# Kernel tuning notes

Hardware: AMD Instinct MI355X
Metric: run time of the kernel (lower is better)

The kernel has to match this reference:

```python
import jax, jax.numpy as jnp
import numpy as np

HUGE = jnp.float32(1e31)   # ops.HUGE_INT
EPS = 1e-20
B, AN = 1024, 256
D = 256            # emb_dim
HD = 512           # history_dim
AD = 2 * D         # action_dim
NE, NR = 100000, 400


def setup_inputs() -> dict:
    key = jax.random.key(0)
    ks = jax.random.split(key, 12)
    e = jax.random.randint(ks[0], (B,), 0, NE)
    q = jax.random.randint(ks[1], (B,), 0, NR)
    hstate = jax.random.normal(ks[2], (B, HD), dtype=jnp.float32)
    r_space = jax.random.randint(ks[3], (B, AN), 0, NR)
    e_space = jax.random.randint(ks[4], (B, AN), 0, NE)
    # binary action mask; guarantee at least one valid action per row
    action_mask = (jax.random.uniform(ks[5], (B, AN)) > 0.2).astype(jnp.float32)
    action_mask = action_mask.at[:, 0].set(1.0)
    entity_emb = jax.random.normal(ks[6], (NE, D), dtype=jnp.float32) * 0.02
    relation_emb = jax.random.normal(ks[7], (NR, D), dtype=jnp.float32) * 0.02
    W1 = jax.random.normal(ks[8], (2 * D + HD, AD), dtype=jnp.float32) * (1.0 / np.sqrt(2 * D + HD))
    b1 = jnp.zeros((AD,), dtype=jnp.float32)
    W2 = jax.random.normal(ks[9], (AD, AD), dtype=jnp.float32) * (1.0 / np.sqrt(AD))
    b2 = jnp.zeros((AD,), dtype=jnp.float32)
    return {"e": e, "q": q, "hstate": hstate, "r_space": r_space,
            "e_space": e_space, "action_mask": action_mask,
            "entity_emb": entity_emb, "relation_emb": relation_emb,
            "W1": W1, "b1": b1, "W2": W2, "b2": b2}


def reference(e, q, hstate, r_space, e_space, action_mask,
              entity_emb, relation_emb, W1, b1, W2, b2):
    Q = relation_emb[q]                       # [B, D]
    E = entity_emb[e]                         # [B, D]
    X = jnp.concatenate([E, hstate, Q], axis=-1)          # [B, 2D+HD]
    X = jax.nn.relu(X @ W1 + b1)                          # [B, AD]
    X2 = X @ W2 + b2                                      # [B, AD]
    # action embeddings: [rel_emb[r]; ent_emb[e]] per padded action slot
    A = jnp.concatenate([relation_emb[r_space], entity_emb[e_space]], axis=-1)  # [B, AN, AD]
    scores = jnp.einsum('bad,bd->ba', A, X2) - (1.0 - action_mask) * HUGE      # [B, AN]
    action_dist = jax.nn.softmax(scores, axis=-1)
    entropy = -jnp.sum(action_dist * jnp.log(jnp.clip(action_dist, EPS)), axis=-1)  # [B]
    return action_dist, entropy
```

## Files before the change

kernel.cpp:

```cpp
#include <hip/hip_runtime.h>
#include <math.h>

#define NB   1024
#define NACT 256
#define DIM  256
#define HDIM 512
#define ADIM 512
#define KTOT 1024
#define NE   100000
#define NR   400
#define NRP  448
#define NCAT 704

typedef __attribute__((ext_vector_type(8))) short bf16x8;
typedef __attribute__((ext_vector_type(4))) float f32x4;

__device__ __forceinline__ unsigned short f2bf(float f) {
    unsigned int u = __float_as_uint(f);
    u += 0x7FFF + ((u >> 16) & 1);
    return (unsigned short)(u >> 16);
}
__device__ __forceinline__ ushort4 cvt4(float4 v) {
    ushort4 o = {f2bf(v.x), f2bf(v.y), f2bf(v.z), f2bf(v.w)};
    return o;
}

__global__ __launch_bounds__(256) void prep_kernel(
    const float* __restrict__ W1, const float* __restrict__ W2,
    const float* __restrict__ rel, const float* __restrict__ b2,
    ushort* __restrict__ W1T, ushort* __restrict__ Bcat,
    ushort* __restrict__ W2lowbf, ushort* __restrict__ relbf,
    float* __restrict__ cvec)
{
    const int blk = blockIdx.x, tid = threadIdx.x;
    if (blk < 160) {
        __shared__ float t[64][68];
        const float* in; ushort* out; int Kd, k0, n0, rowbase;
        if (blk < 128) {
            in = W1; out = W1T; Kd = 1024;
            k0 = (blk >> 3) * 64; n0 = (blk & 7) * 64; rowbase = n0;
        } else {
            const int l = blk - 128;
            in = W2; out = Bcat; Kd = 512;
            k0 = (l >> 2) * 64; n0 = 256 + (l & 3) * 64; rowbase = n0 - 256;
        }
        const int kr = tid >> 2, c = tid & 3;
        #pragma unroll
        for (int j = 0; j < 4; ++j) {
            const float4 v = *(const float4*)(in + (size_t)(k0 + kr) * ADIM + n0 + c * 16 + j * 4);
            *(float4*)&t[kr][c * 16 + j * 4] = v;
        }
        __syncthreads();
        const int nr = tid >> 2;
        ushort tmp[16];
        #pragma unroll
        for (int kk = 0; kk < 16; ++kk) tmp[kk] = f2bf(t[c * 16 + kk][nr]);
        *(uint4*)(out + (size_t)(rowbase + nr) * Kd + k0 + c * 16)     = *(uint4*)&tmp[0];
        *(uint4*)(out + (size_t)(rowbase + nr) * Kd + k0 + c * 16 + 8) = *(uint4*)&tmp[8];
    } else if (blk < 288) {
        const int l = blk - 160;
        const int row = l * 4 + (tid >> 6);
        const int d4  = tid & 63;
        const float4 v = *(const float4*)(W2 + (size_t)row * ADIM + d4 * 4);
        *(ushort4*)(W2lowbf + (size_t)row * DIM + d4 * 4) = cvt4(v);
    } else if (blk < 388) {
        const int j = (blk - 288) * 256 + tid;
        ((ushort4*)relbf)[j] = cvt4(((const float4*)rel)[j]);
    } else {
        const int r = (blk - 388) * 256 + tid;
        if (r < NRP) {
            const int rr = (r < NR) ? r : (NR - 1);
            const float* a = rel + (size_t)rr * DIM;
            float s = 0.f;
            for (int d = 0; d < DIM; d += 4) {
                const float4 av = *(const float4*)(a + d);
                const float4 bv = *(const float4*)(b2 + d);
                s += av.x * bv.x + av.y * bv.y + av.z * bv.z + av.w * bv.w;
            }
            cvec[r] = s;
        }
    }
}

__global__ __launch_bounds__(256) void mega2_kernel(
    const float* __restrict__ ent, const float* __restrict__ rel,
    const float* __restrict__ hstate,
    const int* __restrict__ e, const int* __restrict__ q,
    const ushort* __restrict__ W1T, const ushort* __restrict__ relbf,
    const ushort* __restrict__ W2lowbf,
    ushort* __restrict__ Bcat, float* __restrict__ Hpart)
{
    __shared__ __align__(16) ushort Als[64][40];
    __shared__ __align__(16) ushort Bls[64][40];
    const int blk = blockIdx.x, tid = threadIdx.x;
    const int wave = tid >> 6, lane = tid & 63;
    const int qq   = lane >> 4, l15 = lane & 15;
    const int sm   = tid >> 2, sc = tid & 3;

    f32x4 acc[4];
    #pragma unroll
    for (int mt = 0; mt < 4; ++mt) acc[mt] = (f32x4){0.f, 0.f, 0.f, 0.f};

    if (blk < 56) {
        const int n0 = (blk & 7) * 64;
        const int m0 = (blk >> 3) * 64;
        const int arow = (m0 + sm < NR) ? (m0 + sm) : (NR - 1);
        const uint4* ga = (const uint4*)(relbf + (size_t)arow * DIM) + sc;
        const uint4* gb = (const uint4*)(W2lowbf + (size_t)(n0 + sm) * DIM) + sc;
        uint4 pa = ga[0], pb = gb[0];
        for (int it = 0; it < DIM / 32; ++it) {
            *(uint4*)&Als[sm][sc * 8] = pa;
            *(uint4*)&Bls[sm][sc * 8] = pb;
            __syncthreads();
            if (it + 1 < DIM / 32) { pa = ga[(it + 1) * 4]; pb = gb[(it + 1) * 4]; }
            const bf16x8 bfrag = *(const bf16x8*)&Bls[wave * 16 + l15][qq * 8];
            #pragma unroll
            for (int mt = 0; mt < 4; ++mt) {
                const bf16x8 afrag = *(const bf16x8*)&Als[mt * 16 + l15][qq * 8];
                acc[mt] = __builtin_amdgcn_mfma_f32_16x16x32_bf16(afrag, bfrag, acc[mt], 0, 0, 0);
            }
            __syncthreads();
        }
        const int n = n0 + wave * 16 + l15;
        #pragma unroll
        for (int mt = 0; mt < 4; ++mt)
            #pragma unroll
            for (int r = 0; r < 4; ++r) {
                const int m = m0 + mt * 16 + qq * 4 + r;
                Bcat[(size_t)(256 + m) * ADIM + n] = f2bf(acc[mt][r]);
            }
        return;
    }

    const int g  = blk - 56;
    const int n0 = (g & 7) * 64;
    const int m0 = ((g >> 3) & 15) * 64;
    const int z  = g >> 7;
    const int kbase = z * 256;
    const int kofs  = sc * 8;

    const int row = m0 + sm;
    const float* abase;
    if (z == 0)      abase = ent + (size_t)e[row] * DIM;
    else if (z == 3) abase = rel + (size_t)q[row] * DIM;
    else             abase = hstate + (size_t)row * HDIM + (kbase - DIM);
    const uint4* gb = (const uint4*)(W1T + (size_t)(n0 + sm) * KTOT + kbase) + sc;

    float4 pa0 = *(const float4*)(abase + kofs);
    float4 pa1 = *(const float4*)(abase + kofs + 4);
    uint4  pb  = gb[0];

    for (int it = 0; it < 8; ++it) {
        ushort t8[8];
        t8[0] = f2bf(pa0.x); t8[1] = f2bf(pa0.y); t8[2] = f2bf(pa0.z); t8[3] = f2bf(pa0.w);
        t8[4] = f2bf(pa1.x); t8[5] = f2bf(pa1.y); t8[6] = f2bf(pa1.z); t8[7] = f2bf(pa1.w);
        *(uint4*)&Als[sm][sc * 8] = *(uint4*)t8;
        *(uint4*)&Bls[sm][sc * 8] = pb;
        __syncthreads();
        if (it + 1 < 8) {
            const int lofs = (it + 1) * 32 + kofs;
            pa0 = *(const float4*)(abase + lofs);
            pa1 = *(const float4*)(abase + lofs + 4);
            pb  = gb[(it + 1) * 4];
        }
        const bf16x8 bfrag = *(const bf16x8*)&Bls[wave * 16 + l15][qq * 8];
        #pragma unroll
        for (int mt = 0; mt < 4; ++mt) {
            const bf16x8 afrag = *(const bf16x8*)&Als[mt * 16 + l15][qq * 8];
            acc[mt] = __builtin_amdgcn_mfma_f32_16x16x32_bf16(afrag, bfrag, acc[mt], 0, 0, 0);
        }
        __syncthreads();
    }
    float* dst = Hpart + (size_t)z * NB * ADIM;
    const int n = n0 + wave * 16 + l15;
    #pragma unroll
    for (int mt = 0; mt < 4; ++mt)
        #pragma unroll
        for (int r = 0; r < 4; ++r) {
            const int m = m0 + mt * 16 + qq * 4 + r;
            dst[(size_t)m * ADIM + n] = acc[mt][r];
        }
}

__global__ __launch_bounds__(256) void reduce_x(
    const float* __restrict__ Hpart, const float* __restrict__ b1,
    ushort* __restrict__ Xbf)
{
    const int i = blockIdx.x * 256 + threadIdx.x;
    const int col4 = i & (ADIM / 4 - 1);
    float4 s = ((const float4*)b1)[col4];
    #pragma unroll
    for (int z = 0; z < 4; ++z) {
        const float4 h = ((const float4*)(Hpart + (size_t)z * NB * ADIM))[i];
        s.x += h.x; s.y += h.y; s.z += h.z; s.w += h.w;
    }
    s.x = fmaxf(s.x, 0.f); s.y = fmaxf(s.y, 0.f);
    s.z = fmaxf(s.z, 0.f); s.w = fmaxf(s.w, 0.f);
    ((ushort4*)Xbf)[i] = cvt4(s);
}

__global__ __launch_bounds__(256) void gemm2big(
    const ushort* __restrict__ Xbf, const ushort* __restrict__ Bcat,
    const float* __restrict__ b2, const float* __restrict__ cvec,
    float* __restrict__ X2upPart, float* __restrict__ RtabPart)
{
    __shared__ __align__(16) ushort Als[64][40];
    __shared__ __align__(16) ushort Bls[64][40];
    const int tid  = threadIdx.x;
    const int n0   = blockIdx.x * 64;
    const int m0   = blockIdx.y * 64;
    const int z    = blockIdx.z;
    const int kb   = z * 256;
    const int wave = tid >> 6, lane = tid & 63;
    const int qq   = lane >> 4, l15 = lane & 15;
    const int sm   = tid >> 2, sc = tid & 3;

    const uint4* gap = (const uint4*)(Xbf  + (size_t)(m0 + sm) * ADIM + kb) + sc;
    const uint4* gbp = (const uint4*)(Bcat + (size_t)(n0 + sm) * ADIM + kb) + sc;

    f32x4 acc[4];
    #pragma unroll
    for (int mt = 0; mt < 4; ++mt) acc[mt] = (f32x4){0.f, 0.f, 0.f, 0.f};

    uint4 pa = gap[0], pb = gbp[0];
    for (int it = 0; it < 8; ++it) {
        *(uint4*)&Als[sm][sc * 8] = pa;
        *(uint4*)&Bls[sm][sc * 8] = pb;
        __syncthreads();
        if (it + 1 < 8) { pa = gap[(it + 1) * 4]; pb = gbp[(it + 1) * 4]; }
        const bf16x8 bfrag = *(const bf16x8*)&Bls[wave * 16 + l15][qq * 8];
        #pragma unroll
        for (int mt = 0; mt < 4; ++mt) {
            const bf16x8 afrag = *(const bf16x8*)&Als[mt * 16 + l15][qq * 8];
            acc[mt] = __builtin_amdgcn_mfma_f32_16x16x32_bf16(afrag, bfrag, acc[mt], 0, 0, 0);
        }
        __syncthreads();
    }
    const int n = n0 + wave * 16 + l15;
    const float extra = (z == 0) ? ((n < 256) ? b2[256 + n] : cvec[n - 256]) : 0.0f;
    #pragma unroll
    for (int mt = 0; mt < 4; ++mt)
        #pragma unroll
        for (int r = 0; r < 4; ++r) {
            const int m = m0 + mt * 16 + qq * 4 + r;
            const float v = acc[mt][r] + extra;
            if (n < 256) X2upPart[(size_t)z * NB * DIM + (size_t)m * DIM + n] = v;
            else         RtabPart[(size_t)z * NB * NRP + (size_t)m * NRP + (n - 256)] = v;
        }
}

__global__ __launch_bounds__(512) void scores_kernel(
    const int* __restrict__ r_space, const int* __restrict__ e_space,
    const float* __restrict__ amask,
    const float* __restrict__ ent,
    const float* __restrict__ RtabPart, const float* __restrict__ X2upPart,
    float* __restrict__ dist_out, float* __restrict__ ent_out)
{
    const int b    = blockIdx.x;
    const int tid  = threadIdx.x;
    const int wave = tid >> 6;
    const int lane = tid & 63;
    const int qw   = tid >> 4;
    const int ql   = tid & 15;

    __shared__ float xs[DIM];
    __shared__ float rtab[NRP];
    __shared__ float sc[NACT];
    __shared__ int   eidx[NACT];
    __shared__ int   ridx[NACT];
    __shared__ float red1[8], red2[8], red3[8];

    if (tid < NACT) eidx[tid] = e_space[(size_t)b * NACT + tid];
    else            ridx[tid - NACT] = r_space[(size_t)b * NACT + tid - NACT];
    if (tid < 112) {
        const float4 v0 = ((const float4*)(RtabPart + (size_t)b * NRP))[tid];
        const float4 v1 = ((const float4*)(RtabPart + (size_t)NB * NRP + (size_t)b * NRP))[tid];
        float4 s; s.x = v0.x + v1.x; s.y = v0.y + v1.y; s.z = v0.z + v1.z; s.w = v0.w + v1.w;
        ((float4*)rtab)[tid] = s;
    } else if (tid >= 128 && tid < 192) {
        const int j = tid - 128;
        float4 v0 = ((const float4*)(X2upPart + (size_t)b * DIM))[j];
        const float4 v1 = ((const float4*)(X2upPart + (size_t)NB * DIM + (size_t)b * DIM))[j];
        v0.x += v1.x; v0.y += v1.y; v0.z += v1.z; v0.w += v1.w;
        ((float4*)xs)[j] = v0;
    }
    __syncthreads();

    const float4* xv = ((const float4*)xs) + ql * 4;
    const float4 x0 = xv[0], x1 = xv[1], x2 = xv[2], x3 = xv[3];

    const float4* er = (const float4*)(ent + (size_t)eidx[qw] * DIM) + ql * 4;
    float4 e0 = er[0], e1 = er[1], e2 = er[2], e3 = er[3];

    #pragma unroll
    for (int g = 0; g < 8; ++g) {
        const float4 f0 = e0, f1 = e1, f2 = e2, f3 = e3;
        if (g + 1 < 8) {
            const float4* ern = (const float4*)(ent + (size_t)eidx[(g + 1) * 32 + qw] * DIM) + ql * 4;
            e0 = ern[0]; e1 = ern[1]; e2 = ern[2]; e3 = ern[3];
        }
        float p = f0.x * x0.x + f0.y * x0.y + f0.z * x0.z + f0.w * x0.w
                + f1.x * x1.x + f1.y * x1.y + f1.z * x1.z + f1.w * x1.w
                + f2.x * x2.x + f2.y * x2.y + f2.z * x2.z + f2.w * x2.w
                + f3.x * x3.x + f3.y * x3.y + f3.z * x3.z + f3.w * x3.w;
        p += __shfl_xor(p, 1);
        p += __shfl_xor(p, 2);
        p += __shfl_xor(p, 4);
        p += __shfl_xor(p, 8);
        if (ql == 0) {
            const int a = g * 32 + qw;
            sc[a] = p + rtab[ridx[a]];
        }
    }
    __syncthreads();

    float s = -3.0e38f;
    if (tid < NACT) {
        const float m = amask[(size_t)b * NACT + tid];
        s = sc[tid] - (1.0f - m) * 1e31f;
    }

    float mx = s;
    #pragma unroll
    for (int off = 32; off; off >>= 1) mx = fmaxf(mx, __shfl_xor(mx, off));
    if (lane == 0) red1[wave] = mx;
    __syncthreads();
    mx = fmaxf(fmaxf(fmaxf(red1[0], red1[1]), fmaxf(red1[2], red1[3])),
               fmaxf(fmaxf(red1[4], red1[5]), fmaxf(red1[6], red1[7])));

    const float ex = (tid < NACT) ? expf(s - mx) : 0.0f;
    float sum = ex;
    #pragma unroll
    for (int off = 32; off; off >>= 1) sum += __shfl_xor(sum, off);
    if (lane == 0) red2[wave] = sum;
    __syncthreads();
    sum = ((red2[0] + red2[1]) + (red2[2] + red2[3]))
        + ((red2[4] + red2[5]) + (red2[6] + red2[7]));

    const float d = ex / sum;
    if (tid < NACT) dist_out[(size_t)b * NACT + tid] = d;

    float t = (tid < NACT) ? d * logf(fmaxf(d, 1e-20f)) : 0.0f;
    #pragma unroll
    for (int off = 32; off; off >>= 1) t += __shfl_xor(t, off);
    if (lane == 0) red3[wave] = t;
    __syncthreads();
    if (tid == 0)
        ent_out[b] = -(((red3[0] + red3[1]) + (red3[2] + red3[3]))
                     + ((red3[4] + red3[5]) + (red3[6] + red3[7])));
}

extern "C" void kernel_launch(void* const* d_in, const int* in_sizes, int n_in,
                              void* d_out, int out_size, void* d_ws, size_t ws_size,
                              hipStream_t stream) {
    const int*   e       = (const int*)d_in[0];
    const int*   q       = (const int*)d_in[1];
    const float* hstate  = (const float*)d_in[2];
    const int*   r_space = (const int*)d_in[3];
    const int*   e_space = (const int*)d_in[4];
    const float* amask   = (const float*)d_in[5];
    const float* ent     = (const float*)d_in[6];
    const float* rel     = (const float*)d_in[7];
    const float* W1      = (const float*)d_in[8];
    const float* b1      = (const float*)d_in[9];
    const float* W2      = (const float*)d_in[10];
    const float* b2      = (const float*)d_in[11];

    ushort* W1T    = (ushort*)d_ws;
    ushort* Bcat   = W1T    + (size_t)ADIM * KTOT;
    ushort* W2low  = Bcat   + (size_t)NCAT * ADIM;
    ushort* relbf  = W2low  + (size_t)ADIM * DIM;
    float*  cvec   = (float*)(relbf + (size_t)NR * DIM);
    float*  Hpart  = cvec   + NRP;
    ushort* Xbf    = (ushort*)(Hpart + (size_t)4 * NB * ADIM);
    float*  X2upP  = (float*)(Xbf + (size_t)NB * ADIM);
    float*  RtabP  = X2upP  + (size_t)2 * NB * DIM;
    float*  dist   = (float*)d_out;
    float*  entr   = dist + (size_t)NB * NACT;

    prep_kernel<<<390, 256, 0, stream>>>(W1, W2, rel, b2, W1T, Bcat, W2low, relbf, cvec);
    mega2_kernel<<<568, 256, 0, stream>>>(ent, rel, hstate, e, q, W1T, relbf, W2low, Bcat, Hpart);
    reduce_x<<<512, 256, 0, stream>>>(Hpart, b1, Xbf);
    gemm2big<<<dim3(11, 16, 2), 256, 0, stream>>>(Xbf, Bcat, b2, cvec, X2upP, RtabP);
    scores_kernel<<<NB, 512, 0, stream>>>(
        r_space, e_space, amask, ent, RtabP, X2upP, dist, entr);
}
```

Measured before the change: 217.3 us.

## Remove split-K in both MLP GEMMs and fuse bias/relu epilogue

The first GEMM's four-way K split is replaced by a single block that walks the full K=1024, so the bias, relu and bf16 conversion happen in its epilogue. This drops the partial-sum buffer and the separate reduce_x launch. The second GEMM also loses its two-way K split, so scores_kernel reads the final values directly instead of summing partials. The cost is far fewer blocks (184 and 176 instead of 568 and 352) with longer serial K loops, which may underfill the GPU's compute units.

```diff
diff --git a/kernel.cpp b/kernel.cpp
--- a/kernel.cpp
+++ b/kernel.cpp
@@ -87,8 +87,8 @@
     const float* __restrict__ hstate,
     const int* __restrict__ e, const int* __restrict__ q,
     const ushort* __restrict__ W1T, const ushort* __restrict__ relbf,
-    const ushort* __restrict__ W2lowbf,
-    ushort* __restrict__ Bcat, float* __restrict__ Hpart)
+    const ushort* __restrict__ W2lowbf, const float* __restrict__ b1,
+    ushort* __restrict__ Bcat, ushort* __restrict__ Xbf)
 {
     __shared__ __align__(16) ushort Als[64][40];
     __shared__ __align__(16) ushort Bls[64][40];
@@ -134,34 +134,35 @@
 
     const int g  = blk - 56;
     const int n0 = (g & 7) * 64;
-    const int m0 = ((g >> 3) & 15) * 64;
-    const int z  = g >> 7;
-    const int kbase = z * 256;
-    const int kofs  = sc * 8;
+    const int m0 = (g >> 3) * 64;
+    const int kofs = sc * 8;
 
     const int row = m0 + sm;
-    const float* abase;
-    if (z == 0)      abase = ent + (size_t)e[row] * DIM;
-    else if (z == 3) abase = rel + (size_t)q[row] * DIM;
-    else             abase = hstate + (size_t)row * HDIM + (kbase - DIM);
-    const uint4* gb = (const uint4*)(W1T + (size_t)(n0 + sm) * KTOT + kbase) + sc;
-
-    float4 pa0 = *(const float4*)(abase + kofs);
-    float4 pa1 = *(const float4*)(abase + kofs + 4);
-    uint4  pb  = gb[0];
-
-    for (int it = 0; it < 8; ++it) {
+    const float* entb = ent + (size_t)e[row] * DIM;
+    const float* hb   = hstate + (size_t)row * HDIM;
+    const float* relb = rel + (size_t)q[row] * DIM;
+    const uint4* gb   = (const uint4*)(W1T + (size_t)(n0 + sm) * KTOT);
+
+    const float* ab0 = entb;
+    float4 pa0 = *(const float4*)(ab0 + kofs);
+    float4 pa1 = *(const float4*)(ab0 + kofs + 4);
+    uint4  pb  = gb[sc];
+
+    for (int it = 0; it < 32; ++it) {
         ushort t8[8];
         t8[0] = f2bf(pa0.x); t8[1] = f2bf(pa0.y); t8[2] = f2bf(pa0.z); t8[3] = f2bf(pa0.w);
         t8[4] = f2bf(pa1.x); t8[5] = f2bf(pa1.y); t8[6] = f2bf(pa1.z); t8[7] = f2bf(pa1.w);
         *(uint4*)&Als[sm][sc * 8] = *(uint4*)t8;
         *(uint4*)&Bls[sm][sc * 8] = pb;
         __syncthreads();
-        if (it + 1 < 8) {
-            const int lofs = (it + 1) * 32 + kofs;
-            pa0 = *(const float4*)(abase + lofs);
-            pa1 = *(const float4*)(abase + lofs + 4);
-            pb  = gb[(it + 1) * 4];
+        if (it + 1 < 32) {
+            const int kb = (it + 1) * 32;
+            const float* ab = (kb < 256) ? (entb + kb)
+                             : (kb < 768) ? (hb + (kb - 256))
+                             : (relb + (kb - 768));
+            pa0 = *(const float4*)(ab + kofs);
+            pa1 = *(const float4*)(ab + kofs + 4);
+            pb  = gb[(it + 1) * 4 + sc];
         }
         const bf16x8 bfrag = *(const bf16x8*)&Bls[wave * 16 + l15][qq * 8];
         #pragma unroll
@@ -171,63 +172,44 @@
         }
         __syncthreads();
     }
-    float* dst = Hpart + (size_t)z * NB * ADIM;
     const int n = n0 + wave * 16 + l15;
+    const float bias = b1[n];
     #pragma unroll
     for (int mt = 0; mt < 4; ++mt)
         #pragma unroll
         for (int r = 0; r < 4; ++r) {
             const int m = m0 + mt * 16 + qq * 4 + r;
-            dst[(size_t)m * ADIM + n] = acc[mt][r];
-        }
-}
-
-__global__ __launch_bounds__(256) void reduce_x(
-    const float* __restrict__ Hpart, const float* __restrict__ b1,
-    ushort* __restrict__ Xbf)
-{
-    const int i = blockIdx.x * 256 + threadIdx.x;
-    const int col4 = i & (ADIM / 4 - 1);
-    float4 s = ((const float4*)b1)[col4];
-    #pragma unroll
-    for (int z = 0; z < 4; ++z) {
-        const float4 h = ((const float4*)(Hpart + (size_t)z * NB * ADIM))[i];
-        s.x += h.x; s.y += h.y; s.z += h.z; s.w += h.w;
-    }
-    s.x = fmaxf(s.x, 0.f); s.y = fmaxf(s.y, 0.f);
-    s.z = fmaxf(s.z, 0.f); s.w = fmaxf(s.w, 0.f);
-    ((ushort4*)Xbf)[i] = cvt4(s);
+            Xbf[(size_t)m * ADIM + n] = f2bf(fmaxf(acc[mt][r] + bias, 0.f));
+        }
 }
 
 __global__ __launch_bounds__(256) void gemm2big(
     const ushort* __restrict__ Xbf, const ushort* __restrict__ Bcat,
     const float* __restrict__ b2, const float* __restrict__ cvec,
-    float* __restrict__ X2upPart, float* __restrict__ RtabPart)
+    float* __restrict__ X2up, float* __restrict__ Rtab)
 {
     __shared__ __align__(16) ushort Als[64][40];
     __shared__ __align__(16) ushort Bls[64][40];
     const int tid  = threadIdx.x;
     const int n0   = blockIdx.x * 64;
     const int m0   = blockIdx.y * 64;
-    const int z    = blockIdx.z;
-    const int kb   = z * 256;
     const int wave = tid >> 6, lane = tid & 63;
     const int qq   = lane >> 4, l15 = lane & 15;
     const int sm   = tid >> 2, sc = tid & 3;
 
-    const uint4* gap = (const uint4*)(Xbf  + (size_t)(m0 + sm) * ADIM + kb) + sc;
-    const uint4* gbp = (const uint4*)(Bcat + (size_t)(n0 + sm) * ADIM + kb) + sc;
+    const uint4* gap = (const uint4*)(Xbf  + (size_t)(m0 + sm) * ADIM) + sc;
+    const uint4* gbp = (const uint4*)(Bcat + (size_t)(n0 + sm) * ADIM) + sc;
 
     f32x4 acc[4];
     #pragma unroll
     for (int mt = 0; mt < 4; ++mt) acc[mt] = (f32x4){0.f, 0.f, 0.f, 0.f};
 
     uint4 pa = gap[0], pb = gbp[0];
-    for (int it = 0; it < 8; ++it) {
+    for (int it = 0; it < 16; ++it) {
         *(uint4*)&Als[sm][sc * 8] = pa;
         *(uint4*)&Bls[sm][sc * 8] = pb;
         __syncthreads();
-        if (it + 1 < 8) { pa = gap[(it + 1) * 4]; pb = gbp[(it + 1) * 4]; }
+        if (it + 1 < 16) { pa = gap[(it + 1) * 4]; pb = gbp[(it + 1) * 4]; }
         const bf16x8 bfrag = *(const bf16x8*)&Bls[wave * 16 + l15][qq * 8];
         #pragma unroll
         for (int mt = 0; mt < 4; ++mt) {
@@ -237,15 +219,15 @@
         __syncthreads();
     }
     const int n = n0 + wave * 16 + l15;
-    const float extra = (z == 0) ? ((n < 256) ? b2[256 + n] : cvec[n - 256]) : 0.0f;
+    const float extra = (n < 256) ? b2[256 + n] : cvec[n - 256];
     #pragma unroll
     for (int mt = 0; mt < 4; ++mt)
         #pragma unroll
         for (int r = 0; r < 4; ++r) {
             const int m = m0 + mt * 16 + qq * 4 + r;
             const float v = acc[mt][r] + extra;
-            if (n < 256) X2upPart[(size_t)z * NB * DIM + (size_t)m * DIM + n] = v;
-            else         RtabPart[(size_t)z * NB * NRP + (size_t)m * NRP + (n - 256)] = v;
+            if (n < 256) X2up[(size_t)m * DIM + n] = v;
+            else         Rtab[(size_t)m * NRP + (n - 256)] = v;
         }
 }
 
@@ -253,7 +235,7 @@
     const int* __restrict__ r_space, const int* __restrict__ e_space,
     const float* __restrict__ amask,
     const float* __restrict__ ent,
-    const float* __restrict__ RtabPart, const float* __restrict__ X2upPart,
+    const float* __restrict__ Rtab, const float* __restrict__ X2up,
     float* __restrict__ dist_out, float* __restrict__ ent_out)
 {
     const int b    = blockIdx.x;
@@ -273,16 +255,10 @@
     if (tid < NACT) eidx[tid] = e_space[(size_t)b * NACT + tid];
     else            ridx[tid - NACT] = r_space[(size_t)b * NACT + tid - NACT];
     if (tid < 112) {
-        const float4 v0 = ((const float4*)(RtabPart + (size_t)b * NRP))[tid];
-        const float4 v1 = ((const float4*)(RtabPart + (size_t)NB * NRP + (size_t)b * NRP))[tid];
-        float4 s; s.x = v0.x + v1.x; s.y = v0.y + v1.y; s.z = v0.z + v1.z; s.w = v0.w + v1.w;
-        ((float4*)rtab)[tid] = s;
+        ((float4*)rtab)[tid] = ((const float4*)(Rtab + (size_t)b * NRP))[tid];
     } else if (tid >= 128 && tid < 192) {
         const int j = tid - 128;
-        float4 v0 = ((const float4*)(X2upPart + (size_t)b * DIM))[j];
-        const float4 v1 = ((const float4*)(X2upPart + (size_t)NB * DIM + (size_t)b * DIM))[j];
-        v0.x += v1.x; v0.y += v1.y; v0.z += v1.z; v0.w += v1.w;
-        ((float4*)xs)[j] = v0;
+        ((float4*)xs)[j] = ((const float4*)(X2up + (size_t)b * DIM))[j];
     }
     __syncthreads();
 
@@ -371,17 +347,15 @@
     ushort* W2low  = Bcat   + (size_t)NCAT * ADIM;
     ushort* relbf  = W2low  + (size_t)ADIM * DIM;
     float*  cvec   = (float*)(relbf + (size_t)NR * DIM);
-    float*  Hpart  = cvec   + NRP;
-    ushort* Xbf    = (ushort*)(Hpart + (size_t)4 * NB * ADIM);
-    float*  X2upP  = (float*)(Xbf + (size_t)NB * ADIM);
-    float*  RtabP  = X2upP  + (size_t)2 * NB * DIM;
+    ushort* Xbf    = (ushort*)(cvec + NRP);
+    float*  X2up   = (float*)(Xbf + (size_t)NB * ADIM);
+    float*  Rtab   = X2up   + (size_t)NB * DIM;
     float*  dist   = (float*)d_out;
     float*  entr   = dist + (size_t)NB * NACT;
 
     prep_kernel<<<390, 256, 0, stream>>>(W1, W2, rel, b2, W1T, Bcat, W2low, relbf, cvec);
-    mega2_kernel<<<568, 256, 0, stream>>>(ent, rel, hstate, e, q, W1T, relbf, W2low, Bcat, Hpart);
-    reduce_x<<<512, 256, 0, stream>>>(Hpart, b1, Xbf);
-    gemm2big<<<dim3(11, 16, 2), 256, 0, stream>>>(Xbf, Bcat, b2, cvec, X2upP, RtabP);
+    mega2_kernel<<<184, 256, 0, stream>>>(ent, rel, hstate, e, q, W1T, relbf, W2low, b1, Bcat, Xbf);
+    gemm2big<<<dim3(11, 16), 256, 0, stream>>>(Xbf, Bcat, b2, cvec, X2up, Rtab);
     scores_kernel<<<NB, 512, 0, stream>>>(
-        r_space, e_space, amask, ent, RtabP, X2upP, dist, entr);
-}
+        r_space, e_space, amask, ent, Rtab, X2up, dist, entr);
+}
```

Result: slower. 228.7 us (+5.2%).
